# Optimization experiments

Measured on AMD Instinct MI355X. Metric: run time of the kernel, lower is better.

## Reference

```python
import jax, jax.numpy as jnp
import numpy as np

IN_FEATURES = 512
OUT_FEATURES = 128
KERNEL_DIM = 32
BATCH = 128


def setup_inputs() -> dict:
    key = jax.random.key(0)
    kx, kT = jax.random.split(key)
    x = jax.random.normal(kx, (BATCH, IN_FEATURES), dtype=jnp.float32)
    # nn.Parameter initialized with normal(0, 1)
    T = jax.random.normal(kT, (IN_FEATURES, OUT_FEATURES, KERNEL_DIM), dtype=jnp.float32)
    return {"x": x, "T": T}


def reference(x, T):
    B = x.shape[0]
    in_f, out_f, k_dim = T.shape
    # projection: [B, in] @ [in, out*k] -> [B, out, k]
    m = (x @ T.reshape(in_f, out_f * k_dim)).reshape(B, out_f, k_dim)
    # pairwise L1 distance over kernel dim: [B, B, out]
    # original: M = m[None], M_T = m[:, None]; norm = |M - M_T|.sum(3); o_b = exp(-norm).sum(0) - 1
    norm = jnp.abs(m[None, :, :, :] - m[:, None, :, :]).sum(axis=-1)  # [i=B, j=B, out]
    o_b = jnp.exp(-norm).sum(axis=0) - 1.0  # [B, out] (subtract self-distance term exp(0)=1)
    return jnp.concatenate([x, o_b], axis=1)  # [B, in + out]
```

## Files before the change

kernel.cpp:

```cpp
#include <hip/hip_runtime.h>
#include <hip/hip_fp16.h>

#define IN_F    512
#define NC      4096
#define OUT_COLS 640
#define B_SZ    128
#define MOH_PITCH 72

typedef __attribute__((ext_vector_type(8)))  short bf16x8;
typedef __attribute__((ext_vector_type(16))) float f32x16;

union H2x4  { uint4 u4; __half2 h[4]; };
union FragB { unsigned int u[4]; bf16x8 s; };

static __device__ __forceinline__ unsigned int pack2(float lo, float hi) {
    return (__float_as_uint(lo) >> 16) | (__float_as_uint(hi) & 0xFFFF0000u);
}
static __device__ __forceinline__ __half2 habs2_(__half2 v) {
    unsigned int u = *(unsigned int*)&v & 0x7FFF7FFFu;
    return *(__half2*)&u;
}

__global__ __launch_bounds__(256) void prep_kernel(
    const float* __restrict__ x, float* __restrict__ out,
    unsigned short* __restrict__ xa)
{
    const int g = blockIdx.x * 256 + threadIdx.x;
    const int b = g >> 7, c4 = g & 127;
    float4 v = ((const float4*)x)[g];
    *(float4*)(out + b * OUT_COLS + c4 * 4) = v;
    const int slot = ((b >> 5) * 32 + (c4 >> 2)) * 64 + ((c4 >> 1) & 1) * 32 + (b & 31);
    uint2 pv; pv.x = pack2(v.x, v.y); pv.y = pack2(v.z, v.w);
    *(uint2*)(xa + (size_t)slot * 8 + (c4 & 1) * 4) = pv;
}

__global__ __launch_bounds__(1024, 8) void fused_kernel(
    const unsigned short* __restrict__ xa,
    const float* __restrict__ T,
    float* __restrict__ out)
{
    __shared__ __align__(16) char smem[65536];
    float*  red  = (float*)smem;
    __half* moh  = (__half*)smem;
    float*  psum = (float*)(smem + 18432);

    const int tid    = threadIdx.x;
    const int lane   = tid & 63;
    const int w      = tid >> 6;
    const int o      = blockIdx.x & 127;
    const int jhalf  = blockIdx.x >> 7;
    const int mt     = w & 3;
    const int kg     = w >> 2;
    const int col    = lane & 31;
    const int half32 = lane >> 5;

    f32x16 acc = {0.f,0.f,0.f,0.f,0.f,0.f,0.f,0.f,0.f,0.f,0.f,0.f,0.f,0.f,0.f,0.f};
    const unsigned short* pa = xa + ((size_t)(mt * 32 + kg * 8) * 64 + lane) * 8;
    const float* pb = T + (size_t)(kg * 128 + half32 * 8) * NC + o * 32 + col;
    #pragma unroll
    for (int ch = 0; ch < 8; ++ch) {
        bf16x8 af = *(const bf16x8*)(pa + (size_t)ch * 512);
        const float* tb = pb + (size_t)ch * 16 * NC;
        float b0 = tb[0*NC], b1 = tb[1*NC], b2 = tb[2*NC], b3 = tb[3*NC];
        float b4 = tb[4*NC], b5 = tb[5*NC], b6 = tb[6*NC], b7 = tb[7*NC];
        FragB bf;
        bf.u[0] = pack2(b0, b1); bf.u[1] = pack2(b2, b3);
        bf.u[2] = pack2(b4, b5); bf.u[3] = pack2(b6, b7);
        acc = __builtin_amdgcn_mfma_f32_32x32x16_bf16(af, bf.s, acc, 0, 0, 0);
    }
    {
        float* rd = red + kg * 4096 + mt * 1024 + col;
        #pragma unroll
        for (int r = 0; r < 16; ++r) {
            int row = (r & 3) + 8 * (r >> 2) + 4 * half32;
            rd[row * 32] = acc[r];
        }
    }
    __syncthreads();

    float4 s;
    {
        const int e = tid * 4;
        s = *(const float4*)&red[e];
        #pragma unroll
        for (int p = 1; p < 4; ++p) {
            float4 v2 = *(const float4*)&red[p * 4096 + e];
            s.x += v2.x; s.y += v2.y; s.z += v2.z; s.w += v2.w;
        }
    }
    __syncthreads();
    {
        const int e = tid * 4;
        const int mtt = e >> 10, row = (e >> 5) & 31, c0 = e & 31;
        __half2 lo = __floats2half2_rn(s.x, s.y);
        __half2 hi = __floats2half2_rn(s.z, s.w);
        uint2 w2; w2.x = *(unsigned int*)&lo; w2.y = *(unsigned int*)&hi;
        *(uint2*)&moh[(mtt * 32 + row) * MOH_PITCH + c0] = w2;
    }
    __syncthreads();

    const int jj5 = tid & 31;
    const int isl = tid >> 5;
    const int j0  = jhalf * 64 + jj5;

    __half2 mj0[16], mj1[16];
    #pragma unroll
    for (int k16 = 0; k16 < 4; ++k16) {
        H2x4 a, b;
        a.u4 = *(const uint4*)&moh[j0 * MOH_PITCH + k16 * 8];
        b.u4 = *(const uint4*)&moh[(j0 + 32) * MOH_PITCH + k16 * 8];
        #pragma unroll
        for (int h = 0; h < 4; ++h) { mj0[k16*4+h] = a.h[h]; mj1[k16*4+h] = b.h[h]; }
    }

    float s0 = 0.f, s1 = 0.f;
    #pragma unroll
    for (int ii = 0; ii < 4; ++ii) {
        const int i = isl * 4 + ii;
        __half2 n0 = __float2half2_rn(0.f), n1 = __float2half2_rn(0.f);
        #pragma unroll
        for (int k16 = 0; k16 < 4; ++k16) {
            H2x4 mi; mi.u4 = *(const uint4*)&moh[i * MOH_PITCH + k16 * 8];
            #pragma unroll
            for (int h = 0; h < 4; ++h) {
                n0 = __hadd2(n0, habs2_(__hsub2(mj0[k16*4+h], mi.h[h])));
                n1 = __hadd2(n1, habs2_(__hsub2(mj1[k16*4+h], mi.h[h])));
            }
        }
        float2 f0 = __half22float2(n0), f1 = __half22float2(n1);
        s0 += __expf(-(f0.x + f0.y));
        s1 += __expf(-(f1.x + f1.y));
    }
    psum[jj5 * 33 + isl]        = s0;
    psum[1056 + jj5 * 33 + isl] = s1;
    __syncthreads();
    if (tid < 64) {
        int jsel = tid >> 5, jj = tid & 31;
        float tot = 0.f;
        #pragma unroll
        for (int u = 0; u < 32; ++u) tot += psum[jsel * 1056 + jj * 33 + u];
        out[(jhalf * 64 + jsel * 32 + jj) * OUT_COLS + IN_F + o] = tot - 1.0f;
    }
}

extern "C" void kernel_launch(void* const* d_in, const int* in_sizes, int n_in,
                              void* d_out, int out_size, void* d_ws, size_t ws_size,
                              hipStream_t stream) {
    const float* x = (const float*)d_in[0];
    const float* T = (const float*)d_in[1];
    float* out = (float*)d_out;
    unsigned short* xa = (unsigned short*)d_ws;

    prep_kernel<<<64, 256, 0, stream>>>(x, out, xa);
    fused_kernel<<<256, 1024, 0, stream>>>(xa, T, out);
}
```

Measured before the change: 69.48 us.

## Use 8 MFMA waves with deeper K, separate smem buffers, swizzle moh layout

The projection now runs on only 8 of the 16 waves, each covering a 256-long K range in 16 MFMA steps, so the cross-wave reduction sums two partials instead of four. Because the buffers are now separate shared arrays, one barrier between the reduction and the half-precision store is dropped. The moh rows use an XOR swizzle on 8-element column groups to reduce LDS bank conflicts in the pairwise-distance reads. The cost is that half the waves sit idle during the GEMM phase, which lengthens its serial MFMA and load chain per wave.

```diff
diff --git a/kernel.cpp b/kernel.cpp
--- a/kernel.cpp
+++ b/kernel.cpp
@@ -4,7 +4,6 @@
 #define IN_F    512
 #define NC      4096
 #define OUT_COLS 640
-#define B_SZ    128
 #define MOH_PITCH 72
 
 typedef __attribute__((ext_vector_type(8)))  short bf16x8;
@@ -39,36 +38,35 @@
     const float* __restrict__ T,
     float* __restrict__ out)
 {
-    __shared__ __align__(16) char smem[65536];
-    float*  red  = (float*)smem;
-    __half* moh  = (__half*)smem;
-    float*  psum = (float*)(smem + 18432);
+    __shared__ float red[2 * 4096];
+    __shared__ __align__(16) __half moh[128 * MOH_PITCH];
+    __shared__ float psum[2 * 1056];
 
     const int tid    = threadIdx.x;
     const int lane   = tid & 63;
     const int w      = tid >> 6;
     const int o      = blockIdx.x & 127;
     const int jhalf  = blockIdx.x >> 7;
-    const int mt     = w & 3;
-    const int kg     = w >> 2;
     const int col    = lane & 31;
     const int half32 = lane >> 5;
 
-    f32x16 acc = {0.f,0.f,0.f,0.f,0.f,0.f,0.f,0.f,0.f,0.f,0.f,0.f,0.f,0.f,0.f,0.f};
-    const unsigned short* pa = xa + ((size_t)(mt * 32 + kg * 8) * 64 + lane) * 8;
-    const float* pb = T + (size_t)(kg * 128 + half32 * 8) * NC + o * 32 + col;
-    #pragma unroll
-    for (int ch = 0; ch < 8; ++ch) {
-        bf16x8 af = *(const bf16x8*)(pa + (size_t)ch * 512);
-        const float* tb = pb + (size_t)ch * 16 * NC;
-        float b0 = tb[0*NC], b1 = tb[1*NC], b2 = tb[2*NC], b3 = tb[3*NC];
-        float b4 = tb[4*NC], b5 = tb[5*NC], b6 = tb[6*NC], b7 = tb[7*NC];
-        FragB bf;
-        bf.u[0] = pack2(b0, b1); bf.u[1] = pack2(b2, b3);
-        bf.u[2] = pack2(b4, b5); bf.u[3] = pack2(b6, b7);
-        acc = __builtin_amdgcn_mfma_f32_32x32x16_bf16(af, bf.s, acc, 0, 0, 0);
-    }
-    {
+    if (w < 8) {
+        const int mt = w & 3;
+        const int kg = w >> 2;
+        f32x16 acc = {0.f,0.f,0.f,0.f,0.f,0.f,0.f,0.f,0.f,0.f,0.f,0.f,0.f,0.f,0.f,0.f};
+        const unsigned short* pa = xa + ((size_t)(mt * 32 + kg * 16) * 64 + lane) * 8;
+        const float* pb = T + (size_t)(kg * 256 + half32 * 8) * NC + o * 32 + col;
+        #pragma unroll
+        for (int ch = 0; ch < 16; ++ch) {
+            bf16x8 af = *(const bf16x8*)(pa + (size_t)ch * 512);
+            const float* tb = pb + (size_t)ch * 16 * NC;
+            float b0 = tb[0*NC], b1 = tb[1*NC], b2 = tb[2*NC], b3 = tb[3*NC];
+            float b4 = tb[4*NC], b5 = tb[5*NC], b6 = tb[6*NC], b7 = tb[7*NC];
+            FragB bf;
+            bf.u[0] = pack2(b0, b1); bf.u[1] = pack2(b2, b3);
+            bf.u[2] = pack2(b4, b5); bf.u[3] = pack2(b6, b7);
+            acc = __builtin_amdgcn_mfma_f32_32x32x16_bf16(af, bf.s, acc, 0, 0, 0);
+        }
         float* rd = red + kg * 4096 + mt * 1024 + col;
         #pragma unroll
         for (int r = 0; r < 16; ++r) {
@@ -78,24 +76,18 @@
     }
     __syncthreads();
 
-    float4 s;
     {
         const int e = tid * 4;
-        s = *(const float4*)&red[e];
-        #pragma unroll
-        for (int p = 1; p < 4; ++p) {
-            float4 v2 = *(const float4*)&red[p * 4096 + e];
-            s.x += v2.x; s.y += v2.y; s.z += v2.z; s.w += v2.w;
-        }
-    }
-    __syncthreads();
-    {
-        const int e = tid * 4;
-        const int mtt = e >> 10, row = (e >> 5) & 31, c0 = e & 31;
+        float4 s  = *(const float4*)&red[e];
+        float4 p  = *(const float4*)&red[4096 + e];
+        s.x += p.x; s.y += p.y; s.z += p.z; s.w += p.w;
+        const int mtt = e >> 10, rin = (e >> 5) & 31, c0 = e & 31;
+        const int row = mtt * 32 + rin;
+        const int colp = ((c0 >> 3) ^ ((row >> 3) & 3)) * 8 + (c0 & 7);
         __half2 lo = __floats2half2_rn(s.x, s.y);
         __half2 hi = __floats2half2_rn(s.z, s.w);
         uint2 w2; w2.x = *(unsigned int*)&lo; w2.y = *(unsigned int*)&hi;
-        *(uint2*)&moh[(mtt * 32 + row) * MOH_PITCH + c0] = w2;
+        *(uint2*)&moh[row * MOH_PITCH + colp] = w2;
     }
     __syncthreads();
 
@@ -104,11 +96,12 @@
     const int j0  = jhalf * 64 + jj5;
 
     __half2 mj0[16], mj1[16];
+    const int t0 = (j0 >> 3) & 3;
     #pragma unroll
     for (int k16 = 0; k16 < 4; ++k16) {
         H2x4 a, b;
-        a.u4 = *(const uint4*)&moh[j0 * MOH_PITCH + k16 * 8];
-        b.u4 = *(const uint4*)&moh[(j0 + 32) * MOH_PITCH + k16 * 8];
+        a.u4 = *(const uint4*)&moh[j0 * MOH_PITCH + (k16 ^ t0) * 8];
+        b.u4 = *(const uint4*)&moh[(j0 + 32) * MOH_PITCH + (k16 ^ t0) * 8];
         #pragma unroll
         for (int h = 0; h < 4; ++h) { mj0[k16*4+h] = a.h[h]; mj1[k16*4+h] = b.h[h]; }
     }
@@ -117,10 +110,11 @@
     #pragma unroll
     for (int ii = 0; ii < 4; ++ii) {
         const int i = isl * 4 + ii;
+        const int ti = (i >> 3) & 3;
         __half2 n0 = __float2half2_rn(0.f), n1 = __float2half2_rn(0.f);
         #pragma unroll
         for (int k16 = 0; k16 < 4; ++k16) {
-            H2x4 mi; mi.u4 = *(const uint4*)&moh[i * MOH_PITCH + k16 * 8];
+            H2x4 mi; mi.u4 = *(const uint4*)&moh[i * MOH_PITCH + (k16 ^ ti) * 8];
             #pragma unroll
             for (int h = 0; h < 4; ++h) {
                 n0 = __hadd2(n0, habs2_(__hsub2(mj0[k16*4+h], mi.h[h])));
```

Measured after the change: 70.87 us. +2.0%, slower.
